# Optimization experiments

Measured on AMD Instinct MI355X. Metric: run time of the kernel, lower is better.

Reference implementation:

```python
import jax, jax.numpy as jnp
import numpy as np

B, G, C, K = 16, 2048, 128, 16


def setup_inputs() -> dict:
    key = jax.random.key(0)
    k1, k2, k3, k4 = jax.random.split(key, 4)
    xyz = jax.random.normal(k1, (B, G, 3), dtype=jnp.float32)
    feat = jax.random.normal(k2, (B, G, C), dtype=jnp.float32)
    # MLP params: Linear(C->C) -> GELU -> Linear(C->C)
    W1 = jax.random.normal(k3, (C, C), dtype=jnp.float32) * 0.02
    b1 = jnp.zeros((C,), dtype=jnp.float32)
    W2 = jax.random.normal(k4, (C, C), dtype=jnp.float32) * 0.02
    b2 = jnp.zeros((C,), dtype=jnp.float32)
    return {"xyz": xyz, "feat": feat, "W1": W1, "b1": b1, "W2": W2, "b2": b2}


def _knn_idx(xyz, k):
    # squared pairwise distances [B,G,G]; ranking identical to cdist (sqrt monotone)
    sq = jnp.sum(xyz * xyz, axis=-1)  # [B,G]
    d2 = sq[:, :, None] + sq[:, None, :] - 2.0 * jnp.einsum("bgd,bhd->bgh", xyz, xyz)
    _, idx = jax.lax.top_k(-d2, k)  # smallest distances
    return idx  # [B,G,k]


def reference(xyz, feat, W1, b1, W2, b2):
    idx = _knn_idx(xyz, K)                                   # [B,G,K]
    # gather neighbor features: feat[b, idx[b,g,k], :] -> [B,G,K,C]
    neigh = jnp.take_along_axis(feat[:, None, :, :], idx[..., None], axis=2)
    pooled = jnp.sqrt(jnp.sum(neigh * neigh, axis=-2))       # L2 norm over K -> [B,G,C]
    h = jax.nn.gelu(pooled @ W1 + b1, approximate=False)
    return h @ W2 + b2
```

## Files before the change

### kernel.cpp

```cpp
#include <hip/hip_runtime.h>
#include <math.h>

#define Bn 16
#define Gn 2048
#define Cn 128
#define Kn 16
#define QB 32
#define AS 136

typedef __attribute__((ext_vector_type(8))) short bf16x8;
typedef __attribute__((ext_vector_type(4))) float f32x4;

__device__ __forceinline__ unsigned short f2bf(float x) {
    unsigned int u = __float_as_uint(x);
    unsigned int r = (u + 0x7fffu + ((u >> 16) & 1u)) >> 16;
    return (unsigned short)r;
}
__device__ __forceinline__ float bf2f(unsigned short h) {
    return __uint_as_float(((unsigned int)h) << 16);
}

__device__ __forceinline__ float med3f(float a, float b, float c) {
#if __has_builtin(__builtin_amdgcn_fmed3f)
    return __builtin_amdgcn_fmed3f(a, b, c);
#else
    return fmaxf(fminf(a, b), fminf(fmaxf(a, b), c));
#endif
}

__device__ __forceinline__ float dist2(const float4 me, const float4 p) {
    float dot = fmaf(me.z, p.z, fmaf(me.y, p.y, me.x * p.x));
    return fmaf(-2.0f, dot, me.w + p.w);
}

__device__ __forceinline__ void ins16(float (&d)[16], float v) {
    float prev = d[0];
    d[0] = fminf(d[0], v);
    #pragma unroll
    for (int t = 1; t < 16; ++t) { float cur = d[t]; d[t] = med3f(v, prev, cur); prev = cur; }
}

__device__ __forceinline__ void merge16(float (&d)[16]) {
    #pragma unroll
    for (int m = 1; m < 16; m <<= 1) {
        #pragma unroll
        for (int t = 0; t < 8; ++t) {
            float sa = __shfl_xor(d[15 - t], m);
            float sb = __shfl_xor(d[t], m);
            d[t]      = fminf(d[t], sa);
            d[15 - t] = fminf(d[15 - t], sb);
        }
        #pragma unroll
        for (int k = 8; k; k >>= 1) {
            #pragma unroll
            for (int t = 0; t < 16; ++t)
                if (!(t & k)) {
                    float lo = fminf(d[t], d[t + k]);
                    float hi = fmaxf(d[t], d[t + k]);
                    d[t] = lo; d[t + k] = hi;
                }
        }
    }
}

__device__ __forceinline__ float gelu_exact(float x) {
    return 0.5f * x * (1.0f + erff(x * 0.70710678118654752440f));
}

__global__ __launch_bounds__(256) void prep_w(const float* __restrict__ W1,
                                              const float* __restrict__ W2,
                                              unsigned short* __restrict__ ws) {
    int t = blockIdx.x * 256 + threadIdx.x;
    if (t < 16384) {
        int k = t >> 7, n = t & 127;
        float w = W1[t];
        unsigned short h = f2bf(w);
        unsigned short l = f2bf(w - bf2f(h));
        ws[n * 128 + k]          = h;
        ws[16384 + n * 128 + k]  = l;
        w = W2[t];
        h = f2bf(w);
        l = f2bf(w - bf2f(h));
        ws[32768 + n * 128 + k]  = h;
        ws[49152 + n * 128 + k]  = l;
    }
}

__global__ __launch_bounds__(512) void fused_kernel(const float* __restrict__ xyz,
                                                    const float* __restrict__ feat,
                                                    const float* __restrict__ b1,
                                                    const float* __restrict__ b2,
                                                    const unsigned short* __restrict__ wt,
                                                    float* __restrict__ out) {
    __shared__ __align__(16) float smem0[8704];
    float4* pts = reinterpret_cast<float4*>(smem0);
    unsigned short* Ahi = reinterpret_cast<unsigned short*>(smem0);
    unsigned short* Alo = Ahi + QB * AS;
    unsigned short* outb = reinterpret_cast<unsigned short*>(smem0) + 16384;
    unsigned short* tieb = outb + QB * 16;

    const int x     = blockIdx.x;
    const int b     = x & 15;
    const int chunk = x >> 4;
    const int tid   = threadIdx.x;
    const int lane  = tid & 63;
    const int w     = tid >> 6;
    const int sub   = lane & 15;
    const int qg    = lane >> 4;
    const int q     = w * 4 + qg;
    const int g     = chunk * QB + q;

    const float* xb = xyz + (size_t)b * Gn * 3;
    for (int i = tid; i < Gn; i += 512) {
        float px = xb[i * 3 + 0], py = xb[i * 3 + 1], pz = xb[i * 3 + 2];
        pts[i] = make_float4(px, py, pz, px * px + py * py + pz * pz);
    }
    __syncthreads();

    const float4 me = pts[g];
    const int base = sub << 7;
    const int c    = (37 * sub) & 127;

    float d[16];
    #pragma unroll
    for (int t = 0; t < 16; ++t) d[t] = INFINITY;
    for (int j = 0; j < 32; j += 2) {
        float4 p0 = pts[base + ((j + 0 + c) & 127)];
        float4 p1 = pts[base + ((j + 1 + c) & 127)];
        ins16(d, dist2(me, p0));
        ins16(d, dist2(me, p1));
    }
    merge16(d);
    const float T0 = d[15];

    unsigned mw[4];
    #pragma unroll
    for (int wd = 0; wd < 4; ++wd) {
        unsigned m = 0;
        #pragma unroll
        for (int j = 0; j < 32; j += 2) {
            int t0 = wd * 32 + j;
            float4 p0 = pts[base + ((t0 + 0 + c) & 127)];
            float4 p1 = pts[base + ((t0 + 1 + c) & 127)];
            m |= (dist2(me, p0) <= T0) ? (1u << (j + 0)) : 0u;
            m |= (dist2(me, p1) <= T0) ? (1u << (j + 1)) : 0u;
        }
        mw[wd] = m;
    }
    unsigned long long blo = mw[0] | ((unsigned long long)mw[1] << 32);
    unsigned long long bhi = mw[2] | ((unsigned long long)mw[3] << 32);

    #pragma unroll
    for (int t = 0; t < 16; ++t) d[t] = INFINITY;
    {
        unsigned long long m = blo;
        while (m) {
            int p = __builtin_ctzll(m); m &= m - 1;
            int h = base + ((p + c) & 127);
            ins16(d, dist2(me, pts[h]));
        }
        m = bhi;
        while (m) {
            int p = 64 + __builtin_ctzll(m); m &= m - 1;
            int h = base + ((p + c) & 127);
            ins16(d, dist2(me, pts[h]));
        }
    }
    merge16(d);
    const float T = d[15];

    int myc = __popcll(blo) + __popcll(bhi);
    int mymax = myc;
    #pragma unroll
    for (int m = 1; m < 16; m <<= 1) {
        int o = __shfl_xor(mymax, m);
        mymax = (o > mymax) ? o : mymax;
    }
    const unsigned lowm = (1u << sub) - 1;
    const int shft = lane & 48;
    int nl = 0, nt = 0;
    for (int i = 0; i < mymax; ++i) {
        int h = 0; float v = INFINITY;
        if ((blo | bhi) != 0ull) {
            int p;
            if (blo) { p = __builtin_ctzll(blo); blo &= blo - 1; }
            else     { p = 64 + __builtin_ctzll(bhi); bhi &= bhi - 1; }
            h = base + ((p + c) & 127);
            v = dist2(me, pts[h]);
        }
        bool pl = (v < T), pt = (v == T);
        unsigned long long ml = __ballot(pl);
        unsigned long long mt = __ballot(pt);
        unsigned gml = (unsigned)(ml >> shft) & 0xFFFFu;
        unsigned gmt = (unsigned)(mt >> shft) & 0xFFFFu;
        if (pl) outb[q * 16 + nl + __popc(gml & lowm)] = (unsigned short)h;
        if (pt) { int pp = nt + __popc(gmt & lowm); if (pp < 16) tieb[q * 16 + pp] = (unsigned short)h; }
        nl += __popc(gml);
        nt += __popc(gmt);
    }
    if (sub == 0) {
        int mfill = nl;
        int need  = 16 - mfill;
        int tc = (nt > 16) ? 16 : nt;
        for (int s = 0; s < need; ++s) {
            int best = 0x7fffffff, bp = -1;
            for (int u = 0; u < tc; ++u) {
                int vv = tieb[q * 16 + u];
                if (vv < best) { best = vv; bp = u; }
            }
            if (bp >= 0) { tieb[q * 16 + bp] = 0xFFFF; outb[q * 16 + mfill + s] = (unsigned short)best; }
        }
    }
    __syncthreads();

    const float4* fb4 = (const float4*)(feat + (size_t)b * Gn * Cn);
    const int cl = lane & 31;
    #pragma unroll
    for (int pass = 0; pass < 2; ++pass) {
        int qq = w * 4 + pass * 2 + (lane >> 5);
        float4 a = make_float4(0.f, 0.f, 0.f, 0.f);
        #pragma unroll
        for (int qt = 0; qt < 8; ++qt) {
            int hs[2]; float4 f[2];
            #pragma unroll
            for (int k = 0; k < 2; ++k) hs[k] = outb[qq * 16 + qt * 2 + k];
            #pragma unroll
            for (int k = 0; k < 2; ++k) f[k] = fb4[(size_t)hs[k] * 32 + cl];
            #pragma unroll
            for (int k = 0; k < 2; ++k) {
                a.x = fmaf(f[k].x, f[k].x, a.x);
                a.y = fmaf(f[k].y, f[k].y, a.y);
                a.z = fmaf(f[k].z, f[k].z, a.z);
                a.w = fmaf(f[k].w, f[k].w, a.w);
            }
        }
        float r0 = sqrtf(a.x), r1 = sqrtf(a.y), r2 = sqrtf(a.z), r3 = sqrtf(a.w);
        unsigned short h0 = f2bf(r0), h1 = f2bf(r1), h2 = f2bf(r2), h3 = f2bf(r3);
        ushort4 hv = make_ushort4(h0, h1, h2, h3);
        ushort4 lv = make_ushort4(f2bf(r0 - bf2f(h0)), f2bf(r1 - bf2f(h1)),
                                  f2bf(r2 - bf2f(h2)), f2bf(r3 - bf2f(h3)));
        *(ushort4*)&Ahi[qq * AS + cl * 4] = hv;
        *(ushort4*)&Alo[qq * AS + cl * 4] = lv;
    }
    __syncthreads();

    const int l15  = lane & 15;
    const int kofs = (lane >> 4) * 8;
    const int rowg = (w & 1) * 16;
    const int colg0 = (w >> 1) * 32;
    const unsigned short* wt1h = wt;
    f32x4 acc[2];

    #pragma unroll
    for (int cb = 0; cb < 2; ++cb) {
        float bv = b1[colg0 + cb * 16 + l15];
        acc[cb] = (f32x4){bv, bv, bv, bv};
    }
    #pragma unroll
    for (int kk = 0; kk < 128; kk += 32) {
        bf16x8 ah = *(const bf16x8*)&Ahi[rowg * AS + l15 * AS + kk + kofs];
        bf16x8 al = *(const bf16x8*)&Alo[rowg * AS + l15 * AS + kk + kofs];
        #pragma unroll
        for (int cb = 0; cb < 2; ++cb) {
            const unsigned short* wp = wt1h + (size_t)(colg0 + cb * 16 + l15) * 128 + kk + kofs;
            bf16x8 bh = *(const bf16x8*)wp;
            bf16x8 bl = *(const bf16x8*)(wp + 16384);
            acc[cb] = __builtin_amdgcn_mfma_f32_16x16x32_bf16(ah, bh, acc[cb], 0, 0, 0);
            acc[cb] = __builtin_amdgcn_mfma_f32_16x16x32_bf16(ah, bl, acc[cb], 0, 0, 0);
            acc[cb] = __builtin_amdgcn_mfma_f32_16x16x32_bf16(al, bh, acc[cb], 0, 0, 0);
        }
    }
    __syncthreads();
    #pragma unroll
    for (int cb = 0; cb < 2; ++cb) {
        #pragma unroll
        for (int r = 0; r < 4; ++r) {
            float gv = gelu_exact(acc[cb][r]);
            unsigned short h = f2bf(gv);
            int row = rowg + (lane >> 4) * 4 + r;
            int col = colg0 + cb * 16 + l15;
            Ahi[row * AS + col] = h;
            Alo[row * AS + col] = f2bf(gv - bf2f(h));
        }
    }
    __syncthreads();

    #pragma unroll
    for (int cb = 0; cb < 2; ++cb) {
        float bv = b2[colg0 + cb * 16 + l15];
        acc[cb] = (f32x4){bv, bv, bv, bv};
    }
    #pragma unroll
    for (int kk = 0; kk < 128; kk += 32) {
        bf16x8 ah = *(const bf16x8*)&Ahi[rowg * AS + l15 * AS + kk + kofs];
        bf16x8 al = *(const bf16x8*)&Alo[rowg * AS + l15 * AS + kk + kofs];
        #pragma unroll
        for (int cb = 0; cb < 2; ++cb) {
            const unsigned short* wp = wt1h + 32768 + (size_t)(colg0 + cb * 16 + l15) * 128 + kk + kofs;
            bf16x8 bh = *(const bf16x8*)wp;
            bf16x8 bl = *(const bf16x8*)(wp + 16384);
            acc[cb] = __builtin_amdgcn_mfma_f32_16x16x32_bf16(ah, bh, acc[cb], 0, 0, 0);
            acc[cb] = __builtin_amdgcn_mfma_f32_16x16x32_bf16(ah, bl, acc[cb], 0, 0, 0);
            acc[cb] = __builtin_amdgcn_mfma_f32_16x16x32_bf16(al, bh, acc[cb], 0, 0, 0);
        }
    }
    const size_t orow0 = (size_t)b * Gn + (size_t)chunk * QB + rowg + (lane >> 4) * 4;
    #pragma unroll
    for (int cb = 0; cb < 2; ++cb) {
        #pragma unroll
        for (int r = 0; r < 4; ++r) {
            out[(orow0 + r) * Cn + colg0 + cb * 16 + l15] = acc[cb][r];
        }
    }
}

extern "C" void kernel_launch(void* const* d_in, const int* in_sizes, int n_in,
                              void* d_out, int out_size, void* d_ws, size_t ws_size,
                              hipStream_t stream) {
    const float* xyz  = (const float*)d_in[0];
    const float* feat = (const float*)d_in[1];
    const float* W1   = (const float*)d_in[2];
    const float* b1   = (const float*)d_in[3];
    const float* W2   = (const float*)d_in[4];
    const float* b2   = (const float*)d_in[5];
    float* out = (float*)d_out;
    unsigned short* wt = (unsigned short*)d_ws;

    prep_w<<<64, 256, 0, stream>>>(W1, W2, wt);
    fused_kernel<<<1024, 512, 0, stream>>>(xyz, feat, b1, b2, wt, out);
}
```

Measured before the change: 158.3 us.

## Use interleaved point ownership and cheap 2nd-min group threshold for KNN prefilter

Replaces the per-lane top-16 insertion over 32 sampled points with a running two-smallest tracker using med3, then takes the max across the 16 lanes of the query group as the pruning threshold. The max of 16 per-lane second-minimums is still an upper bound on the 16th nearest distance, so correctness holds, and it avoids the costly 16-slot insertion sort in the first pass. Point ownership changes from contiguous 128-point blocks with a rotated start to an interleaved stride-16 layout, which also changes LDS access patterns. The threshold may be looser, so more candidates can pass the bitmask filter and cost more work later.

Result: slower. 182.6 us (+15.4%).

```diff
diff --git a/kernel.cpp b/kernel.cpp
--- a/kernel.cpp
+++ b/kernel.cpp
@@ -118,51 +118,46 @@
     __syncthreads();
 
     const float4 me = pts[g];
-    const int base = sub << 7;
-    const int c    = (37 * sub) & 127;
-
-    float d[16];
-    #pragma unroll
-    for (int t = 0; t < 16; ++t) d[t] = INFINITY;
-    for (int j = 0; j < 32; j += 2) {
-        float4 p0 = pts[base + ((j + 0 + c) & 127)];
-        float4 p1 = pts[base + ((j + 1 + c) & 127)];
-        ins16(d, dist2(me, p0));
-        ins16(d, dist2(me, p1));
-    }
-    merge16(d);
-    const float T0 = d[15];
+
+    float m1 = INFINITY, m2 = INFINITY;
+    #pragma unroll 8
+    for (int j = 0; j < 32; ++j) {
+        float v = dist2(me, pts[j * 16 + sub]);
+        m2 = med3f(v, m1, m2);
+        m1 = fminf(m1, v);
+    }
+    float T0 = m2;
+    #pragma unroll
+    for (int m = 1; m < 16; m <<= 1) T0 = fmaxf(T0, __shfl_xor(T0, m));
 
     unsigned mw[4];
     #pragma unroll
     for (int wd = 0; wd < 4; ++wd) {
-        unsigned m = 0;
-        #pragma unroll
-        for (int j = 0; j < 32; j += 2) {
-            int t0 = wd * 32 + j;
-            float4 p0 = pts[base + ((t0 + 0 + c) & 127)];
-            float4 p1 = pts[base + ((t0 + 1 + c) & 127)];
-            m |= (dist2(me, p0) <= T0) ? (1u << (j + 0)) : 0u;
-            m |= (dist2(me, p1) <= T0) ? (1u << (j + 1)) : 0u;
-        }
-        mw[wd] = m;
+        unsigned mm = 0;
+        #pragma unroll 8
+        for (int j = 0; j < 32; ++j) {
+            float v = dist2(me, pts[(wd * 32 + j) * 16 + sub]);
+            mm |= (v <= T0) ? (1u << j) : 0u;
+        }
+        mw[wd] = mm;
     }
     unsigned long long blo = mw[0] | ((unsigned long long)mw[1] << 32);
     unsigned long long bhi = mw[2] | ((unsigned long long)mw[3] << 32);
 
+    float d[16];
     #pragma unroll
     for (int t = 0; t < 16; ++t) d[t] = INFINITY;
     {
         unsigned long long m = blo;
         while (m) {
             int p = __builtin_ctzll(m); m &= m - 1;
-            int h = base + ((p + c) & 127);
+            int h = (p << 4) | sub;
             ins16(d, dist2(me, pts[h]));
         }
         m = bhi;
         while (m) {
             int p = 64 + __builtin_ctzll(m); m &= m - 1;
-            int h = base + ((p + c) & 127);
+            int h = (p << 4) | sub;
             ins16(d, dist2(me, pts[h]));
         }
     }
@@ -185,7 +180,7 @@
             int p;
             if (blo) { p = __builtin_ctzll(blo); blo &= blo - 1; }
             else     { p = 64 + __builtin_ctzll(bhi); bhi &= bhi - 1; }
-            h = base + ((p + c) & 127);
+            h = (p << 4) | sub;
             v = dist2(me, pts[h]);
         }
         bool pl = (v < T), pt = (v == T);
```
